# Optimization experiments

Measured on AMD Instinct MI355X. Metric: run time of the kernel, lower is better.

Reference implementation:

```python
import jax, jax.numpy as jnp
import numpy as np

N_HEADS = 32
N_KV = 8
HEAD_DIM = 128
EPS = 1e-5

def _rope(t, fr, fi):
    # t: [b,s,h,hd] -> pairs [b,s,h,hd/2,2]; fr/fi: [s,hd/2]
    tp = t.astype(jnp.float32).reshape(*t.shape[:-1], HEAD_DIM // 2, 2)
    a, b = tp[..., 0], tp[..., 1]
    fr = fr[None, :, None, :]
    fi = fi[None, :, None, :]
    out = jnp.stack([a * fr - b * fi, a * fi + b * fr], axis=-1)
    return out.reshape(t.shape).astype(t.dtype)

def _rmsnorm(t):
    tf = t.astype(jnp.float32)
    return (tf * jax.lax.rsqrt(jnp.mean(tf * tf, axis=-1, keepdims=True) + EPS)).astype(t.dtype)

def setup_inputs() -> dict:
    key = jax.random.key(0)
    ks = jax.random.split(key, 5)
    b, s, dim = 1, 2048, 4096
    x = jax.random.normal(ks[0], (b, s, dim), dtype=jnp.float32) * 0.02
    wq = jax.random.normal(ks[1], (dim, dim), dtype=jnp.float32) * 0.02
    wk = jax.random.normal(ks[2], (N_KV * HEAD_DIM, dim), dtype=jnp.float32) * 0.02
    wv = jax.random.normal(ks[3], (N_KV * HEAD_DIM, dim), dtype=jnp.float32) * 0.02
    wo = jax.random.normal(ks[4], (dim, dim), dtype=jnp.float32) * 0.02
    # RoPE freqs, llama-style theta=10000
    inv = 1.0 / (10000.0 ** (np.arange(0, HEAD_DIM, 2, dtype=np.float32) / HEAD_DIM))
    ang = np.outer(np.arange(s, dtype=np.float32), inv)  # [s, hd/2]
    freqs_cis = jnp.asarray(np.stack([np.cos(ang), np.sin(ang)], axis=-1))  # [s, hd/2, 2]
    # causal additive mask
    mask = jnp.where(jnp.tril(jnp.ones((s, s), dtype=bool)), 0.0, -1e30).astype(jnp.float32)
    return {"x": x, "wq": wq, "wk": wk, "wv": wv, "wo": wo,
            "freqs_cis": freqs_cis, "mask": mask, "start_pos": 0}

def reference(x, wq, wk, wv, wo, freqs_cis, mask, start_pos):
    b, s, dim = x.shape
    n_rep = N_HEADS // N_KV
    xq = jnp.einsum('bsd,ed->bse', x, wq).reshape(b, s, N_HEADS, HEAD_DIM)
    xk = jnp.einsum('bsd,ed->bse', x, wk).reshape(b, s, N_KV, HEAD_DIM)
    xv = jnp.einsum('bsd,ed->bse', x, wv).reshape(b, s, N_KV, HEAD_DIM)
    fr, fi = freqs_cis[..., 0], freqs_cis[..., 1]
    xq = _rope(xq, fr, fi)
    xk = _rope(xk, fr, fi)
    xq = _rmsnorm(xq)
    xk = _rmsnorm(xk)
    # start_pos=0 prefill: KV cache write/read is identity on xk/xv
    q = xq.transpose(0, 2, 1, 3).reshape(b, N_KV, n_rep, s, HEAD_DIM)  # grouped query heads
    k = xk.transpose(0, 2, 1, 3)  # [b, n_kv, s, hd]
    v = xv.transpose(0, 2, 1, 3)
    scores = jnp.einsum('bkrsd,bktd->bkrst', q, k) / np.sqrt(HEAD_DIM)
    scores = scores + mask[None, None, None, :, :]
    probs = jax.nn.softmax(scores, axis=-1)
    o = jnp.einsum('bkrst,bktd->bkrsd', probs, v)
    o = o.reshape(b, N_HEADS, s, HEAD_DIM).transpose(0, 2, 1, 3).reshape(b, s, dim)
    return jnp.einsum('bse,de->bsd', o, wo)
```

## Files before the change

### kernel.cpp

```cpp
#include <hip/hip_runtime.h>
#include <hip/hip_bf16.h>
#include <cstdint>
#include <cstddef>

using u16 = unsigned short;
using u32 = unsigned int;
using u64 = unsigned long long;

typedef __attribute__((ext_vector_type(8))) __bf16 bf16x8;
typedef __attribute__((ext_vector_type(4))) float f32x4;
typedef __attribute__((ext_vector_type(2))) float f32x2;
typedef __attribute__((ext_vector_type(4))) u32 u32x4;

typedef const __attribute__((address_space(1))) void* gas_ptr;
typedef __attribute__((address_space(3))) void* las_ptr;

__device__ __forceinline__ void async_cp16(const void* g, void* l) {
  __builtin_amdgcn_global_load_lds((gas_ptr)g, (las_ptr)l, 16, 0, 0);
}

__device__ __forceinline__ float bf2f(u16 u) {
  u32 v = ((u32)u) << 16;
  return __builtin_bit_cast(float, v);
}
__device__ __forceinline__ u16 f2bf(float f) {
  u32 v = __builtin_bit_cast(u32, f);
  u32 r = (v + 0x7fffu + ((v >> 16) & 1u)) >> 16;
  return (u16)r;
}

__device__ __forceinline__ f32x4 mfma16(bf16x8 a, bf16x8 b, f32x4 c) {
  return __builtin_amdgcn_mfma_f32_16x16x32_bf16(a, b, c, 0, 0, 0);
}

__global__ __launch_bounds__(256) void cvt4(const float* __restrict__ x,
                                            const float* __restrict__ wq,
                                            const float* __restrict__ wk,
                                            const float* __restrict__ wv,
                                            u16* __restrict__ xb,
                                            u16* __restrict__ wqkv) {
  const int B0 = 1048576;
  const int B1 = B0 + 2097152;
  const int B2 = B1 + 524288;
  const int B3 = B2 + 524288;
  int i = blockIdx.x * blockDim.x + threadIdx.x;
  int stride = gridDim.x * blockDim.x;
  for (; i < B3; i += stride) {
    const float* src; u16* dst; int j;
    if (i < B0)      { src = x;  dst = xb;                           j = i; }
    else if (i < B1) { src = wq; dst = wqkv;                         j = i - B0; }
    else if (i < B2) { src = wk; dst = wqkv + (size_t)4096 * 4096;   j = i - B1; }
    else             { src = wv; dst = wqkv + (size_t)5120 * 4096;   j = i - B2; }
    const float4* p = (const float4*)(src + (size_t)j * 8);
    float4 a = p[0], b = p[1];
    union { u16 us[8]; u32x4 v; } o;
    o.us[0] = f2bf(a.x); o.us[1] = f2bf(a.y); o.us[2] = f2bf(a.z); o.us[3] = f2bf(a.w);
    o.us[4] = f2bf(b.x); o.us[5] = f2bf(b.y); o.us[6] = f2bf(b.z); o.us[7] = f2bf(b.w);
    *(u32x4*)(dst + (size_t)j * 8) = o.v;
  }
}

template <int MODE>
__global__ __launch_bounds__(256, 3) void gemm_bt(const u16* __restrict__ A,
                                                  const u16* __restrict__ B,
                                                  void* __restrict__ Cv,
                                                  int M, int N, int K,
                                                  u16* __restrict__ qh,
                                                  u16* __restrict__ khh,
                                                  u16* __restrict__ vt,
                                                  const float* __restrict__ freqs) {
  __shared__ __align__(16) u16 As[128 * 64];
  __shared__ __align__(16) u16 Bs[128 * 64];
  const int tid = threadIdx.x;
  const int wave = tid >> 6, lane = tid & 63;
  const int quad = lane >> 4, c16 = lane & 15;

  const int mb = M >> 7, nb = N >> 7;
  const int per_xcd_n = nb >> 3;
  const int xcd = blockIdx.x & 7, lid = blockIdx.x >> 3;
  const int m_t = lid % mb, n_local = lid / mb;
  const int m0 = m_t * 128, n0 = (xcd * per_xcd_n + n_local) * 128;

  const int wm = (wave & 1) * 64, wn = (wave >> 1) * 64;

  f32x4 acc[4][4] = {};

  const u16* Ab = A + (size_t)m0 * K;
  const u16* Bb = B + (size_t)n0 * K;

  for (int k0 = 0; k0 < K; k0 += 64) {
    __syncthreads();
#pragma unroll
    for (int i = 0; i < 4; ++i) {
      int idx = tid + 256 * i;
      int row = idx >> 3, sg = (idx & 7) ^ (row & 7);
      async_cp16(Ab + (size_t)row * K + k0 + sg * 8, As + (size_t)idx * 8);
    }
#pragma unroll
    for (int i = 0; i < 4; ++i) {
      int idx = tid + 256 * i;
      int row = idx >> 3, sg = (idx & 7) ^ (row & 7);
      async_cp16(Bb + (size_t)row * K + k0 + sg * 8, Bs + (size_t)idx * 8);
    }
    asm volatile("s_waitcnt vmcnt(0)" ::: "memory");
    __syncthreads();

    bf16x8 af[4][2], bfr[4][2];
#pragma unroll
    for (int mt = 0; mt < 4; ++mt) {
      int row = wm + mt * 16 + c16;
#pragma unroll
      for (int c = 0; c < 2; ++c)
        af[mt][c] = *(const bf16x8*)(As + row * 64 + (((c * 4 + quad) ^ (row & 7)) * 8));
    }
#pragma unroll
    for (int nt = 0; nt < 4; ++nt) {
      int row = wn + nt * 16 + c16;
#pragma unroll
      for (int c = 0; c < 2; ++c)
        bfr[nt][c] = *(const bf16x8*)(Bs + row * 64 + (((c * 4 + quad) ^ (row & 7)) * 8));
    }
#pragma unroll
    for (int c = 0; c < 2; ++c)
#pragma unroll
      for (int mt = 0; mt < 4; ++mt)
#pragma unroll
        for (int nt = 0; nt < 4; ++nt)
          acc[mt][nt] = mfma16(af[mt][c], bfr[nt][c], acc[mt][nt]);
  }

  if constexpr (MODE == 1) {
#pragma unroll
    for (int mt = 0; mt < 4; ++mt) {
#pragma unroll
      for (int nt = 0; nt < 4; ++nt) {
#pragma unroll
        for (int r = 0; r < 4; ++r) {
          int gm = m0 + wm + mt * 16 + quad * 4 + r;
          int gn = n0 + wn + nt * 16 + c16;
          ((float*)Cv)[(size_t)gm * N + gn] = acc[mt][nt][r];
        }
      }
    }
  } else {
    __syncthreads();
    float* sums = (float*)As;
    if (n0 < 5120) {
      float ss_arr[4][4];
#pragma unroll
      for (int mt = 0; mt < 4; ++mt) {
#pragma unroll
        for (int r = 0; r < 4; ++r) {
          int s = m0 + wm + mt * 16 + quad * 4 + r;
          const float* fb = freqs + (size_t)s * 128;
          float ssv = 0.0f;
#pragma unroll
          for (int nt = 0; nt < 4; ++nt) {
            int d = wn + nt * 16 + c16;
            float v = acc[mt][nt][r];
            float p = __shfl_xor(v, 1, 64);
            f32x2 ff = *(const f32x2*)(fb + (d & ~1));
            float res = (c16 & 1) ? fmaf(v, ff.x, p * ff.y)
                                  : fmaf(v, ff.x, -p * ff.y);
            acc[mt][nt][r] = res;
            ssv = fmaf(res, res, ssv);
          }
#pragma unroll
          for (int m = 1; m < 16; m <<= 1) ssv += __shfl_xor(ssv, m, 64);
          ss_arr[mt][r] = ssv;
        }
      }
      const int wn_idx = wave >> 1;
      if (c16 == 0) {
#pragma unroll
        for (int mt = 0; mt < 4; ++mt)
#pragma unroll
          for (int r = 0; r < 4; ++r)
            sums[wn_idx * 128 + wm + mt * 16 + quad * 4 + r] = ss_arr[mt][r];
      }
      __syncthreads();
      u16* outb = (n0 < 4096)
                      ? (qh + (size_t)(n0 >> 7) * M * 128)
                      : (khh + (size_t)((n0 - 4096) >> 7) * M * 128);
#pragma unroll
      for (int mt = 0; mt < 4; ++mt) {
#pragma unroll
        for (int r = 0; r < 4; ++r) {
          int rl = wm + mt * 16 + quad * 4 + r;
          float tot = ss_arr[mt][r] + sums[(wn_idx ^ 1) * 128 + rl];
          float scl = rsqrtf(tot * (1.0f / 128.0f) + 1e-5f);
          int s = m0 + rl;
#pragma unroll
          for (int nt = 0; nt < 4; ++nt)
            outb[(size_t)s * 128 + wn + nt * 16 + c16] = f2bf(acc[mt][nt][r] * scl);
        }
      }
    } else {
#pragma unroll
      for (int mt = 0; mt < 4; ++mt) {
#pragma unroll
        for (int nt = 0; nt < 4; ++nt) {
          int dv = (n0 - 5120) + wn + nt * 16 + c16;
          int s0 = m0 + wm + mt * 16 + quad * 4;
          union { u16 us[4]; u64 v; } pk;
#pragma unroll
          for (int r = 0; r < 4; ++r) pk.us[r] = f2bf(acc[mt][nt][r]);
          *(u64*)(vt + (size_t)dv * M + s0) = pk.v;
        }
      }
    }
  }
}

#define SEQ 2048
__global__ __launch_bounds__(512, 2) void attn(const u16* __restrict__ Q,
                                               const u16* __restrict__ Kh,
                                               const u16* __restrict__ VT,
                                               u16* __restrict__ O,
                                               const float* __restrict__ wo,
                                               u16* __restrict__ wob) {
  __shared__ __align__(16) u16 Ks[2][64 * 128];
  __shared__ __align__(16) u16 Vs[2][128 * 64];
  __shared__ __align__(16) u16 Ps[8][32 * 64];
  const int tid = threadIdx.x;
  const int wave = tid >> 6, lane = tid & 63;
  const int quad = lane >> 4, c16 = lane & 15;
  const int bid = blockIdx.x;
  const int hk = bid & 7;
  const int rest = bid >> 3;
  const int hq = rest & 3;
  const int p = rest >> 2;
  const int h = hk * 4 + hq;

  const int wl = wave & 3, grp = wave >> 2;
  const int qt = grp ? p : (15 - p);
  const int q0w = qt * 128 + wl * 32;
  const int kend = (15 - p) * 128 + 128;

  const float sc = 0.12751743f;
  const float B = 16.5f;
  const u16* Kb = Kh + (size_t)hk * SEQ * 128;
  const u16* Vb = VT + (size_t)hk * 128 * SEQ;

  auto stage = [&](int t0, int b) __attribute__((always_inline)) {
#pragma unroll
    for (int i = 0; i < 2; ++i) {
      int idx = tid + 512 * i;
      int row = idx >> 4, sg = (idx & 15) ^ (row & 7);
      async_cp16(Kb + (size_t)(t0 + row) * 128 + sg * 8, &Ks[b][(size_t)idx * 8]);
    }
#pragma unroll
    for (int i = 0; i < 2; ++i) {
      int idx = tid + 512 * i;
      int row = idx >> 3, sg = (idx & 7) ^ (row & 7);
      async_cp16(Vb + (size_t)row * SEQ + t0 + sg * 8, &Vs[b][(size_t)idx * 8]);
    }
  };

  bf16x8 qfr[2][4];
  const u16* qbase = Q + (size_t)h * SEQ * 128;
#pragma unroll
  for (int g = 0; g < 2; ++g)
#pragma unroll
    for (int c = 0; c < 4; ++c)
      qfr[g][c] =
          *(const bf16x8*)(qbase + (size_t)(q0w + g * 16 + c16) * 128 + c * 32 + quad * 8);

  f32x4 o_acc[2][8] = {};
  float lsum[2][4] = {};

  stage(0, 0);

#pragma unroll 1
  for (int t0 = 0; t0 < kend; t0 += 64) {
    const int cur = (t0 >> 6) & 1;
    asm volatile("s_waitcnt vmcnt(0)" ::: "memory");
    __syncthreads();
    if (t0 + 64 < kend) stage(t0 + 64, cur ^ 1);

    if (t0 < q0w + 32) {
      f32x4 sa[2][4] = {};
      __builtin_amdgcn_s_setprio(1);
#pragma unroll
      for (int ct = 0; ct < 4; ++ct) {
        int t = ct * 16 + c16;
        int tbase = t * 128;
        int tsw = t & 7;
#pragma unroll
        for (int c = 0; c < 4; ++c) {
          bf16x8 kf = *(const bf16x8*)(&Ks[cur][tbase + (((c * 4 + quad) ^ tsw) * 8)]);
          sa[0][ct] = mfma16(qfr[0][c], kf, sa[0][ct]);
          sa[1][ct] = mfma16(qfr[1][c], kf, sa[1][ct]);
        }
      }
      __builtin_amdgcn_s_setprio(0);

      const bool diag = (t0 + 64 > q0w);
      auto soft = [&](bool masked) __attribute__((always_inline)) {
#pragma unroll
        for (int g = 0; g < 2; ++g) {
#pragma unroll
          for (int r = 0; r < 4; ++r) {
            int row = g * 16 + quad * 4 + r;
            int row_q = q0w + row;
            int rbase = row * 64;
            int rsw = row & 7;
#pragma unroll
            for (int ct = 0; ct < 4; ++ct) {
              float s = sa[g][ct][r];
              float arg = fmaf(s, sc, -B);
              if (masked) {
                int t_idx = t0 + ct * 16 + c16;
                arg = (t_idx <= row_q) ? arg : -1.0e30f;
              }
              float pe = exp2f(arg);
              lsum[g][r] += pe;
              u32 pb = (__builtin_bit_cast(u32, pe) + 0x8000u) >> 16;
              Ps[wave][rbase + (((ct * 2 + (c16 >> 3)) ^ rsw) * 8) + (c16 & 7)] = (u16)pb;
            }
          }
        }
      };
      if (diag) soft(true); else soft(false);
      asm volatile("s_waitcnt lgkmcnt(0)" ::: "memory");

      __builtin_amdgcn_s_setprio(1);
#pragma unroll
      for (int tc = 0; tc < 2; ++tc) {
        bf16x8 pf[2];
#pragma unroll
        for (int g = 0; g < 2; ++g) {
          int prow = g * 16 + c16;
          pf[g] = *(const bf16x8*)(&Ps[wave][prow * 64 + (((tc * 4 + quad) ^ (prow & 7)) * 8)]);
        }
#pragma unroll
        for (int nt = 0; nt < 8; ++nt) {
          int dl = nt * 16 + c16;
          bf16x8 vf = *(const bf16x8*)(&Vs[cur][dl * 64 + (((tc * 4 + quad) ^ (dl & 7)) * 8)]);
          o_acc[0][nt] = mfma16(pf[0], vf, o_acc[0][nt]);
          o_acc[1][nt] = mfma16(pf[1], vf, o_acc[1][nt]);
        }
      }
      __builtin_amdgcn_s_setprio(0);
    }
  }

#pragma unroll
  for (int g = 0; g < 2; ++g) {
#pragma unroll
    for (int r = 0; r < 4; ++r) {
      float l = lsum[g][r];
#pragma unroll
      for (int m = 1; m < 16; m <<= 1) l += __shfl_xor(l, m, 64);
      float inv = 1.0f / l;
      int s_idx = q0w + g * 16 + quad * 4 + r;
      u16* ob = O + (size_t)s_idx * 4096 + (size_t)h * 128;
#pragma unroll
      for (int nt = 0; nt < 8; ++nt) ob[nt * 16 + c16] = f2bf(o_acc[g][nt][r] * inv);
    }
  }

  {
    const int UNIT = 2341;
    const int N8 = 2097152;
    int su = 16 * p * (p - 1) + (bid & 31) * p;
    int i = su * UNIT + tid;
    int end = su * UNIT + p * UNIT;
    if (end > N8) end = N8;
    for (; i < end; i += 512) {
      const float4* src = (const float4*)(wo + (size_t)i * 8);
      float4 a = src[0], b = src[1];
      union { u16 us[8]; u32x4 v; } o;
      o.us[0] = f2bf(a.x); o.us[1] = f2bf(a.y); o.us[2] = f2bf(a.z); o.us[3] = f2bf(a.w);
      o.us[4] = f2bf(b.x); o.us[5] = f2bf(b.y); o.us[6] = f2bf(b.z); o.us[7] = f2bf(b.w);
      *(u32x4*)(wob + (size_t)i * 8) = o.v;
    }
  }
}

extern "C" void kernel_launch(void* const* d_in, const int* in_sizes, int n_in,
                              void* d_out, int out_size, void* d_ws, size_t ws_size,
                              hipStream_t stream) {
  const float* x  = (const float*)d_in[0];
  const float* wq = (const float*)d_in[1];
  const float* wk = (const float*)d_in[2];
  const float* wv = (const float*)d_in[3];
  const float* wo = (const float*)d_in[4];
  const float* fr = (const float*)d_in[5];
  float* out = (float*)d_out;

  const size_t S = 2048, D = 4096, KV = 1024, NQKV = D + 2 * KV;
  u16* p = (u16*)d_ws;
  u16* xb   = p; p += S * D;
  u16* wqkv = p; p += NQKV * D;
  u16* qh   = p; p += S * D;
  u16* khh  = p; p += S * KV;
  u16* vt   = p; p += KV * S;
  u16* ob   = p; p += S * D;
  u16* wob = wqkv;

  cvt4<<<dim3(2048), dim3(256), 0, stream>>>(x, wq, wk, wv, xb, wqkv);

  gemm_bt<2><<<dim3((S / 128) * (NQKV / 128)), dim3(256), 0, stream>>>(
      xb, wqkv, nullptr, (int)S, (int)NQKV, (int)D, qh, khh, vt, fr);

  attn<<<dim3(256), dim3(512), 0, stream>>>(qh, khh, vt, ob, wo, wob);

  gemm_bt<1><<<dim3((S / 128) * (D / 128)), dim3(256), 0, stream>>>(
      ob, wob, (void*)out, (int)S, (int)D, (int)D,
      nullptr, nullptr, nullptr, nullptr);
}
```

Before: 454.9 us.

## Use 256x256 double-buffered tile GEMM for QKV projection with fused RoPE/RMSNorm

Adds a dedicated QKV-projection kernel that uses 256x256 output tiles with 512 threads and double-buffered async LDS staging split into two k-subphases. Wait counts and barriers are set by hand, and MFMA issue priority is raised while computing. The RoPE and RMSNorm epilogue is adapted to the new wave layout, with each wave covering half a head. The goal is more operand reuse per byte loaded and global loads that overlap compute. The cost is a grid of only 192 blocks (possible load imbalance across CUs) and high register pressure from 128 accumulators per lane.

```diff
diff --git a/kernel.cpp b/kernel.cpp
--- a/kernel.cpp
+++ b/kernel.cpp
@@ -60,15 +60,170 @@
   }
 }
 
-template <int MODE>
-__global__ __launch_bounds__(256, 3) void gemm_bt(const u16* __restrict__ A,
+__global__ __launch_bounds__(512, 2) void gemm256(const u16* __restrict__ A,
                                                   const u16* __restrict__ B,
-                                                  void* __restrict__ Cv,
                                                   int M, int N, int K,
                                                   u16* __restrict__ qh,
                                                   u16* __restrict__ khh,
                                                   u16* __restrict__ vt,
                                                   const float* __restrict__ freqs) {
+  __shared__ __align__(16) u16 As[2][16384];
+  __shared__ __align__(16) u16 Bs[2][16384];
+  const int tid = threadIdx.x;
+  const int wave = tid >> 6, lane = tid & 63;
+  const int quad = lane >> 4, c16 = lane & 15;
+  const int wr = wave >> 2, wc = wave & 3;
+
+  const int mb = M >> 8;
+  const int nb = N >> 8;
+  const int per_xcd_n = nb >> 3;
+  const int xcd = blockIdx.x & 7, lid = blockIdx.x >> 3;
+  const int m_t = lid % mb, n_local = lid / mb;
+  const int m0 = m_t * 256, n0 = (xcd * per_xcd_n + n_local) * 256;
+
+  const u16* Ab = A + (size_t)m0 * K;
+  const u16* Bb = B + (size_t)n0 * K;
+
+  f32x4 acc[8][4] = {};
+
+  auto stageA = [&](int k0, int ks, int b) __attribute__((always_inline)) {
+#pragma unroll
+    for (int i = 0; i < 2; ++i) {
+      int n = tid + 512 * i;
+      int row = n >> 2;
+      int col = k0 + ks * 32 + (((n & 3) ^ (row & 3)) * 8);
+      async_cp16(Ab + (size_t)row * K + col, &As[b][ks * 8192 + n * 8]);
+    }
+  };
+  auto stageB = [&](int k0, int ks, int b) __attribute__((always_inline)) {
+#pragma unroll
+    for (int i = 0; i < 2; ++i) {
+      int n = tid + 512 * i;
+      int row = n >> 2;
+      int col = k0 + ks * 32 + (((n & 3) ^ (row & 3)) * 8);
+      async_cp16(Bb + (size_t)row * K + col, &Bs[b][ks * 8192 + n * 8]);
+    }
+  };
+
+  auto phase_compute = [&](int b, int ks) __attribute__((always_inline)) {
+    bf16x8 af[8], bf[4];
+    const u16* Abase = &As[b][ks * 8192];
+    const u16* Bbase = &Bs[b][ks * 8192];
+#pragma unroll
+    for (int mt = 0; mt < 8; ++mt) {
+      int row = wr * 128 + mt * 16 + c16;
+      af[mt] = *(const bf16x8*)(Abase + row * 32 + ((quad ^ (row & 3)) * 8));
+    }
+#pragma unroll
+    for (int nt = 0; nt < 4; ++nt) {
+      int row = wc * 64 + nt * 16 + c16;
+      bf[nt] = *(const bf16x8*)(Bbase + row * 32 + ((quad ^ (row & 3)) * 8));
+    }
+    __builtin_amdgcn_s_setprio(1);
+#pragma unroll
+    for (int mt = 0; mt < 8; ++mt)
+#pragma unroll
+      for (int nt = 0; nt < 4; ++nt)
+        acc[mt][nt] = mfma16(af[mt], bf[nt], acc[mt][nt]);
+    __builtin_amdgcn_s_setprio(0);
+  };
+
+  const int nk = K >> 6;
+  stageA(0, 0, 0);  stageB(0, 0, 0);
+  stageA(0, 1, 0);  stageB(0, 1, 0);
+  stageA(64, 0, 1); stageB(64, 0, 1);
+
+#pragma unroll 1
+  for (int t = 0; t < nk; ++t) {
+    const int b = t & 1;
+    const int k0 = t << 6;
+    if (t < nk - 1) asm volatile("s_waitcnt vmcnt(8)" ::: "memory");
+    else            asm volatile("s_waitcnt vmcnt(4)" ::: "memory");
+    __builtin_amdgcn_s_barrier();
+    __builtin_amdgcn_sched_barrier(0);
+    if (t + 1 < nk) { stageA(k0 + 64, 1, b ^ 1); stageB(k0 + 64, 1, b ^ 1); }
+    phase_compute(b, 0);
+    if (t < nk - 1) asm volatile("s_waitcnt vmcnt(8)" ::: "memory");
+    else            asm volatile("s_waitcnt vmcnt(0)" ::: "memory");
+    __builtin_amdgcn_s_barrier();
+    __builtin_amdgcn_sched_barrier(0);
+    if (t + 2 < nk) { stageA(k0 + 128, 0, b); stageB(k0 + 128, 0, b); }
+    phase_compute(b, 1);
+  }
+
+  __syncthreads();
+  float* sums = (float*)&As[0][0];
+  if (n0 < 5120) {
+    float ss_arr[8][4];
+    const int dbase = (wc & 1) * 64;
+#pragma unroll
+    for (int mt = 0; mt < 8; ++mt) {
+#pragma unroll
+      for (int r = 0; r < 4; ++r) {
+        int s = m0 + wr * 128 + mt * 16 + quad * 4 + r;
+        const float* fb = freqs + (size_t)s * 128;
+        float ssv = 0.0f;
+#pragma unroll
+        for (int nt = 0; nt < 4; ++nt) {
+          int d = dbase + nt * 16 + c16;
+          float v = acc[mt][nt][r];
+          float p = __shfl_xor(v, 1, 64);
+          f32x2 ff = *(const f32x2*)(fb + (d & ~1));
+          float res = (c16 & 1) ? fmaf(v, ff.x, p * ff.y)
+                                : fmaf(v, ff.x, -p * ff.y);
+          acc[mt][nt][r] = res;
+          ssv = fmaf(res, res, ssv);
+        }
+#pragma unroll
+        for (int m = 1; m < 16; m <<= 1) ssv += __shfl_xor(ssv, m, 64);
+        ss_arr[mt][r] = ssv;
+      }
+    }
+    if (c16 == 0) {
+#pragma unroll
+      for (int mt = 0; mt < 8; ++mt)
+#pragma unroll
+        for (int r = 0; r < 4; ++r)
+          sums[wc * 256 + wr * 128 + mt * 16 + quad * 4 + r] = ss_arr[mt][r];
+    }
+    __syncthreads();
+    const int head_col = n0 + wc * 64;
+    u16* outb = (head_col < 4096)
+                    ? (qh + (size_t)(head_col >> 7) * M * 128)
+                    : (khh + (size_t)((head_col - 4096) >> 7) * M * 128);
+#pragma unroll
+    for (int mt = 0; mt < 8; ++mt) {
+#pragma unroll
+      for (int r = 0; r < 4; ++r) {
+        int rl = wr * 128 + mt * 16 + quad * 4 + r;
+        float tot = ss_arr[mt][r] + sums[(wc ^ 1) * 256 + rl];
+        float scl = rsqrtf(tot * (1.0f / 128.0f) + 1e-5f);
+        int s = m0 + rl;
+#pragma unroll
+        for (int nt = 0; nt < 4; ++nt)
+          outb[(size_t)s * 128 + dbase + nt * 16 + c16] = f2bf(acc[mt][nt][r] * scl);
+      }
+    }
+  } else {
+#pragma unroll
+    for (int mt = 0; mt < 8; ++mt) {
+#pragma unroll
+      for (int nt = 0; nt < 4; ++nt) {
+        int dv = (n0 - 5120) + wc * 64 + nt * 16 + c16;
+        int s0 = m0 + wr * 128 + mt * 16 + quad * 4;
+        union { u16 us[4]; u64 v; } pk;
+#pragma unroll
+        for (int r = 0; r < 4; ++r) pk.us[r] = f2bf(acc[mt][nt][r]);
+        *(u64*)(vt + (size_t)dv * M + s0) = pk.v;
+      }
+    }
+  }
+}
+
+__global__ __launch_bounds__(256, 3) void gemm_out(const u16* __restrict__ A,
+                                                   const u16* __restrict__ B,
+                                                   float* __restrict__ C,
+                                                   int M, int N, int K) {
   __shared__ __align__(16) u16 As[128 * 64];
   __shared__ __align__(16) u16 Bs[128 * 64];
   const int tid = threadIdx.x;
@@ -129,84 +284,15 @@
           acc[mt][nt] = mfma16(af[mt][c], bfr[nt][c], acc[mt][nt]);
   }
 
-  if constexpr (MODE == 1) {
-#pragma unroll
-    for (int mt = 0; mt < 4; ++mt) {
-#pragma unroll
-      for (int nt = 0; nt < 4; ++nt) {
-#pragma unroll
-        for (int r = 0; r < 4; ++r) {
-          int gm = m0 + wm + mt * 16 + quad * 4 + r;
-          int gn = n0 + wn + nt * 16 + c16;
-          ((float*)Cv)[(size_t)gm * N + gn] = acc[mt][nt][r];
-        }
-      }
-    }
-  } else {
-    __syncthreads();
-    float* sums = (float*)As;
-    if (n0 < 5120) {
-      float ss_arr[4][4];
-#pragma unroll
-      for (int mt = 0; mt < 4; ++mt) {
-#pragma unroll
-        for (int r = 0; r < 4; ++r) {
-          int s = m0 + wm + mt * 16 + quad * 4 + r;
-          const float* fb = freqs + (size_t)s * 128;
-          float ssv = 0.0f;
-#pragma unroll
-          for (int nt = 0; nt < 4; ++nt) {
-            int d = wn + nt * 16 + c16;
-            float v = acc[mt][nt][r];
-            float p = __shfl_xor(v, 1, 64);
-            f32x2 ff = *(const f32x2*)(fb + (d & ~1));
-            float res = (c16 & 1) ? fmaf(v, ff.x, p * ff.y)
-                                  : fmaf(v, ff.x, -p * ff.y);
-            acc[mt][nt][r] = res;
-            ssv = fmaf(res, res, ssv);
-          }
-#pragma unroll
-          for (int m = 1; m < 16; m <<= 1) ssv += __shfl_xor(ssv, m, 64);
-          ss_arr[mt][r] = ssv;
-        }
-      }
-      const int wn_idx = wave >> 1;
-      if (c16 == 0) {
-#pragma unroll
-        for (int mt = 0; mt < 4; ++mt)
-#pragma unroll
-          for (int r = 0; r < 4; ++r)
-            sums[wn_idx * 128 + wm + mt * 16 + quad * 4 + r] = ss_arr[mt][r];
-      }
-      __syncthreads();
-      u16* outb = (n0 < 4096)
-                      ? (qh + (size_t)(n0 >> 7) * M * 128)
-                      : (khh + (size_t)((n0 - 4096) >> 7) * M * 128);
-#pragma unroll
-      for (int mt = 0; mt < 4; ++mt) {
-#pragma unroll
-        for (int r = 0; r < 4; ++r) {
-          int rl = wm + mt * 16 + quad * 4 + r;
-          float tot = ss_arr[mt][r] + sums[(wn_idx ^ 1) * 128 + rl];
-          float scl = rsqrtf(tot * (1.0f / 128.0f) + 1e-5f);
-          int s = m0 + rl;
-#pragma unroll
-          for (int nt = 0; nt < 4; ++nt)
-            outb[(size_t)s * 128 + wn + nt * 16 + c16] = f2bf(acc[mt][nt][r] * scl);
-        }
-      }
-    } else {
-#pragma unroll
-      for (int mt = 0; mt < 4; ++mt) {
-#pragma unroll
-        for (int nt = 0; nt < 4; ++nt) {
-          int dv = (n0 - 5120) + wn + nt * 16 + c16;
-          int s0 = m0 + wm + mt * 16 + quad * 4;
-          union { u16 us[4]; u64 v; } pk;
-#pragma unroll
-          for (int r = 0; r < 4; ++r) pk.us[r] = f2bf(acc[mt][nt][r]);
-          *(u64*)(vt + (size_t)dv * M + s0) = pk.v;
-        }
+#pragma unroll
+  for (int mt = 0; mt < 4; ++mt) {
+#pragma unroll
+    for (int nt = 0; nt < 4; ++nt) {
+#pragma unroll
+      for (int r = 0; r < 4; ++r) {
+        int gm = m0 + wm + mt * 16 + quad * 4 + r;
+        int gn = n0 + wn + nt * 16 + c16;
+        C[(size_t)gm * N + gn] = acc[mt][nt][r];
       }
     }
   }
@@ -401,12 +487,11 @@
 
   cvt4<<<dim3(2048), dim3(256), 0, stream>>>(x, wq, wk, wv, xb, wqkv);
 
-  gemm_bt<2><<<dim3((S / 128) * (NQKV / 128)), dim3(256), 0, stream>>>(
-      xb, wqkv, nullptr, (int)S, (int)NQKV, (int)D, qh, khh, vt, fr);
+  gemm256<<<dim3((S / 256) * (NQKV / 256)), dim3(512), 0, stream>>>(
+      xb, wqkv, (int)S, (int)NQKV, (int)D, qh, khh, vt, fr);
 
   attn<<<dim3(256), dim3(512), 0, stream>>>(qh, khh, vt, ob, wo, wob);
 
-  gemm_bt<1><<<dim3((S / 128) * (D / 128)), dim3(256), 0, stream>>>(
-      ob, wob, (void*)out, (int)S, (int)D, (int)D,
-      nullptr, nullptr, nullptr, nullptr);
-}
+  gemm_out<<<dim3((S / 128) * (D / 128)), dim3(256), 0, stream>>>(
+      ob, wob, out, (int)S, (int)D, (int)D);
+}
```

Result: slower. 490.9 us (+7.9%).
